# Kernel optimization log

Measured on AMD Instinct MI355X. Metric: run time of the kernel, lower is better.

Reference implementation:

```python
import jax, jax.numpy as jnp
import numpy as np

N, H, W, C = 8, 64, 64, 256
G, KS = 4, 3
K = KS * KS                      # 9 kernel points (remove_center=False)
GD = C // G                      # 64 channels per group
OM_DIM = int(np.ceil(G * K * 3 / 8) * 8)   # 112 = offsets(72)+mask(36)+pad(4)
STRIDE = PAD = DIL = 1
OFFSET_SCALE = 1.0
SOFTMAX = False


def setup_inputs() -> dict:
    ks = jax.random.split(jax.random.key(0), 6)
    s = 0.02
    return {
        "x": jax.random.normal(ks[0], (N, H * W, C), jnp.float32),
        "shape_h": H,
        "shape_w": W,
        "w_in": jax.random.normal(ks[1], (C, C), jnp.float32) * s,
        "b_in": jnp.zeros((C,), jnp.float32),
        "w_out": jax.random.normal(ks[2], (C, C), jnp.float32) * s,
        "b_out": jnp.zeros((C,), jnp.float32),
        "w_dw": jax.random.normal(ks[3], (KS, KS, 1, C), jnp.float32) * s,  # depthwise HWIO
        "b_dw": jnp.zeros((C,), jnp.float32),
        "w_pw": jax.random.normal(ks[4], (OM_DIM, C), jnp.float32) * s,
        "b_pw": jnp.zeros((OM_DIM,), jnp.float32),
    }


def _deform_sample(xg, px, py, mask):
    # xg: [N, H*W, G, GD]; px/py/mask: [N, H, W, G, K]
    # Bilinear sample with zero padding outside the image, mask-weighted sum over K.
    n_idx = jnp.arange(N)[:, None, None, None, None]
    g_idx = jnp.arange(G)[None, None, None, :, None]
    x0 = jnp.floor(px)
    y0 = jnp.floor(py)
    out = jnp.zeros((N, H, W, G, GD), xg.dtype)
    for dy in (0, 1):
        for dx in (0, 1):
            xi = x0 + dx
            yi = y0 + dy
            wgt = (1.0 - jnp.abs(px - xi)) * (1.0 - jnp.abs(py - yi))
            valid = (xi >= 0) & (xi <= W - 1) & (yi >= 0) & (yi <= H - 1)
            wgt = jnp.where(valid, wgt, 0.0) * mask                     # [N,H,W,G,K]
            flat = (jnp.clip(yi, 0, H - 1) * W + jnp.clip(xi, 0, W - 1)).astype(jnp.int32)
            vals = xg[n_idx, flat, g_idx, :]                            # [N,H,W,G,K,GD]
            out = out + jnp.einsum("nhwgk,nhwgkc->nhwgc", wgt, vals)
    return out


def _forward(x, w_in, b_in, w_out, b_out, w_dw, b_dw, w_pw, b_pw):
    out = x @ w_in.T + b_in                                             # proj_input [N,L,C]
    # offset/mask branch runs on the raw (unprojected) input
    dw = jax.lax.conv_general_dilated(
        x.reshape(N, H, W, C), w_dw, (1, 1), [(PAD, PAD), (PAD, PAD)],
        dimension_numbers=("NHWC", "HWIO", "NHWC"), feature_group_count=C) + b_dw
    om = (dw.reshape(N, H * W, C) @ w_pw.T + b_pw).reshape(N, H, W, OM_DIM)
    off = om[..., : 2 * G * K].reshape(N, H, W, G, K, 2)                # (dx, dy)
    mask = om[..., 2 * G * K : 3 * G * K].reshape(N, H, W, G, K)
    if SOFTMAX:
        mask = jax.nn.softmax(mask, axis=-1)
    # sampling locations in input pixel coordinates (DCNv3 reference points)
    kk = (jnp.arange(KS) - (KS - 1) // 2) * DIL
    kgy, kgx = jnp.meshgrid(kk, kk, indexing="ij")
    kgx = kgx.reshape(-1).astype(x.dtype)                               # [K]
    kgy = kgy.reshape(-1).astype(x.dtype)
    base = (DIL * (KS - 1)) // 2 - PAD
    bx = (jnp.arange(W) * STRIDE + base).astype(x.dtype)
    by = (jnp.arange(H) * STRIDE + base).astype(x.dtype)
    px = bx[None, None, :, None, None] + OFFSET_SCALE * (kgx + off[..., 0])
    py = by[None, :, None, None, None] + OFFSET_SCALE * (kgy + off[..., 1])
    samp = _deform_sample(out.reshape(N, H * W, G, GD), px, py, mask)   # [N,H,W,G,GD]
    return samp.reshape(N, H * W, C) @ w_out.T + b_out                  # proj_output


def reference(x, shape_h, shape_w, w_in, b_in, w_out, b_out, w_dw, b_dw, w_pw, b_pw):
    assert (shape_h, shape_w) == (H, W)
    return _forward(x, w_in, b_in, w_out, b_out, w_dw, b_dw, w_pw, b_pw)
```

## Files before the change

### kernel.cpp

```cpp
#include <hip/hip_runtime.h>

#define HW     4096
#define M_ROWS 32768
#define OMD    112
#define OMP    128

typedef __attribute__((ext_vector_type(8))) short short8;
typedef __attribute__((ext_vector_type(4))) float f32x4;

__device__ inline unsigned short f2bf(float f) {
  union { float f; unsigned int u; } v; v.f = f;
  unsigned int u = v.u;
  u += 0x7fffu + ((u >> 16) & 1u);
  return (unsigned short)(u >> 16);
}
__device__ inline float bf2f(unsigned short h) {
  union { unsigned int u; float f; } v; v.u = ((unsigned int)h) << 16;
  return v.f;
}

__global__ __launch_bounds__(256) void prep_fused(
    const float* __restrict__ x, const float* __restrict__ w_dw,
    const float* __restrict__ b_dw, const float* __restrict__ w_in,
    const float* __restrict__ w_out, const float* __restrict__ w_pw,
    const float* __restrict__ b_pw, unsigned short* __restrict__ xb,
    unsigned short* __restrict__ dwb, unsigned short* __restrict__ wi_b,
    unsigned short* __restrict__ wo_b, unsigned short* __restrict__ wp_b,
    float* __restrict__ bpw_pad) {
  int bid = blockIdx.x;
  int tid = threadIdx.x;
  if (bid < 8192) {
    int idx = bid * 256 + tid;
    int c4 = (idx & 63) * 4;
    int pp = idx >> 6;
    int n = pp >> 12;
    int hw = pp & 4095;
    int h = hw >> 6, w = hw & 63;
    float4 bb = *(const float4*)&b_dw[c4];
    float a0 = bb.x, a1 = bb.y, a2 = bb.z, a3 = bb.w;
#pragma unroll
    for (int ky = 0; ky < 3; ++ky) {
      int iy = h + ky - 1;
      if (iy < 0 || iy > 63) continue;
#pragma unroll
      for (int kx = 0; kx < 3; ++kx) {
        int ix = w + kx - 1;
        if (ix < 0 || ix > 63) continue;
        float4 xv = *(const float4*)&x[((size_t)(n << 12) + iy * 64 + ix) * 256 + c4];
        float4 wv = *(const float4*)&w_dw[(ky * 3 + kx) * 256 + c4];
        a0 += xv.x * wv.x;
        a1 += xv.y * wv.y;
        a2 += xv.z * wv.z;
        a3 += xv.w * wv.w;
      }
    }
    ushort4 o;
    o.x = f2bf(a0); o.y = f2bf(a1); o.z = f2bf(a2); o.w = f2bf(a3);
    *(ushort4*)&dwb[(size_t)pp * 256 + c4] = o;
    float4 cv = *(const float4*)&x[(size_t)pp * 256 + c4];
    ushort4 oc;
    oc.x = f2bf(cv.x); oc.y = f2bf(cv.y); oc.z = f2bf(cv.z); oc.w = f2bf(cv.w);
    *(ushort4*)&xb[(size_t)pp * 256 + c4] = oc;
  } else {
    int idx = (bid - 8192) * 256 + tid;
    if (idx < 65536) {
      wi_b[idx] = f2bf(w_in[idx]);
    } else if (idx < 131072) {
      int i = idx - 65536;
      wo_b[i] = f2bf(w_out[i]);
    } else if (idx < 131072 + OMP * 256) {
      int i = idx - 131072;
      int o = i >> 8;
      wp_b[i] = (o < OMD) ? f2bf(w_pw[i]) : (unsigned short)0;
    } else if (idx < 131072 + OMP * 256 + OMP) {
      int i = idx - (131072 + OMP * 256);
      bpw_pad[i] = (i < OMD) ? b_pw[i] : 0.f;
    }
  }
}

__global__ __launch_bounds__(256) void gemm_mid(
    const unsigned short* __restrict__ dwb, const unsigned short* __restrict__ wp_b,
    const float* __restrict__ bpw, unsigned short* __restrict__ om,
    const unsigned short* __restrict__ xb, const unsigned short* __restrict__ wi_b,
    const float* __restrict__ b_in, unsigned short* __restrict__ vproj) {
  __shared__ __align__(16) unsigned short As[128 * 32];
  __shared__ __align__(16) unsigned short Bs[128 * 32];
  int tid = threadIdx.x;
  int wave = tid >> 6, lane = tid & 63;
  int wr = wave >> 1, wc = wave & 1;

  const unsigned short *A, *W;
  const float* bias;
  unsigned short* Cout;
  int NN, colB;
  size_t rowB;
  int bid = blockIdx.x;
  if (bid < 256) {
    int swz = (bid & 7) * 32 + (bid >> 3);
    A = dwb; W = wp_b; bias = bpw; Cout = om; NN = 128;
    rowB = (size_t)swz * 128; colB = 0;
  } else {
    int b = bid - 256;
    int swz = (b & 7) * 64 + (b >> 3);
    A = xb; W = wi_b; bias = b_in; Cout = vproj; NN = 256;
    rowB = (size_t)(swz >> 1) * 128; colB = (swz & 1) * 128;
  }

  f32x4 acc[4][4];
#pragma unroll
  for (int m = 0; m < 4; ++m)
#pragma unroll
    for (int n = 0; n < 4; ++n) acc[m][n] = (f32x4)(0.f);

  int arow = lane >> 2;
  int acol = (lane & 3) * 8;

  for (int k0 = 0; k0 < 256; k0 += 32) {
#pragma unroll
    for (int jj = 0; jj < 2; ++jj) {
      int j = wave * 2 + jj;
      const unsigned short* ga = A + (rowB + 16 * j + arow) * 256 + k0 + acol;
      __builtin_amdgcn_global_load_lds(
          (const __attribute__((address_space(1))) unsigned int*)ga,
          (__attribute__((address_space(3))) unsigned int*)(As + j * 512),
          16, 0, 0);
      const unsigned short* gb =
          W + ((size_t)(colB + 16 * j + arow)) * 256 + k0 + acol;
      __builtin_amdgcn_global_load_lds(
          (const __attribute__((address_space(1))) unsigned int*)gb,
          (__attribute__((address_space(3))) unsigned int*)(Bs + j * 512),
          16, 0, 0);
    }
    __syncthreads();

    short8 aF[4], bF[4];
#pragma unroll
    for (int m = 0; m < 4; ++m)
      aF[m] = *(const short8*)&As[(wr * 64 + m * 16 + (lane & 15)) * 32 +
                                  (lane >> 4) * 8];
#pragma unroll
    for (int n = 0; n < 4; ++n)
      bF[n] = *(const short8*)&Bs[(wc * 64 + n * 16 + (lane & 15)) * 32 +
                                  (lane >> 4) * 8];
#pragma unroll
    for (int m = 0; m < 4; ++m)
#pragma unroll
      for (int n = 0; n < 4; ++n)
        acc[m][n] = __builtin_amdgcn_mfma_f32_16x16x32_bf16(
            aF[m], bF[n], acc[m][n], 0, 0, 0);
    __syncthreads();
  }

#pragma unroll
  for (int n = 0; n < 4; ++n) {
    int col = colB + wc * 64 + n * 16 + (lane & 15);
    float bv = bias[col];
#pragma unroll
    for (int m = 0; m < 4; ++m) {
#pragma unroll
      for (int j = 0; j < 4; ++j) {
        size_t row = rowB + wr * 64 + m * 16 + (lane >> 4) * 4 + j;
        Cout[row * NN + col] = f2bf(acc[m][n][j] + bv);
      }
    }
  }
}

__global__ __launch_bounds__(256) void deform_sample_v4(
    const unsigned short* __restrict__ vproj, const unsigned short* __restrict__ om,
    unsigned short* __restrict__ samp) {
  __shared__ __align__(16) unsigned short s_v[144 * 128];

  int bid = blockIdx.x;
  int swz = (bid & 7) * 128 + (bid >> 3);
  int n = swz >> 7;
  int t = swz & 127;
  int c0 = (t & 1) << 7;
  int tile = t >> 1;
  int ty0 = (tile >> 3) << 3, tx0 = (tile & 7) << 3;
  int wy0 = ty0 - 2, wx0 = tx0 - 2;

  int tid = threadIdx.x;
  int wave = tid >> 6, lane = tid & 63;

  const unsigned short* vimg = vproj + ((size_t)n << 12) * 256;
#pragma unroll
  for (int i = 0; i < 9; ++i) {
    int cell = i * 16 + (tid >> 4);
    int r = cell / 12, c = cell % 12;
    int gy = min(max(wy0 + r, 0), 63);
    int gx = min(max(wx0 + c, 0), 63);
    const unsigned short* src =
        vimg + (size_t)(gy * 64 + gx) * 256 + c0 + (tid & 15) * 8;
    __builtin_amdgcn_global_load_lds(
        (const __attribute__((address_space(1))) unsigned int*)src,
        (__attribute__((address_space(3))) unsigned int*)(s_v + i * 2048 + wave * 512),
        16, 0, 0);
  }
  __syncthreads();

  int sub = lane & 15;
  int g = (c0 >> 6) + (sub >> 3);
  int chlds = sub * 8;

#pragma unroll
  for (int iter = 0; iter < 4; ++iter) {
    int pl = iter * 16 + wave * 4 + (lane >> 4);
    int py = pl >> 3, pxx = pl & 7;
    int hy = ty0 + py, wx = tx0 + pxx;
    int p = (n << 12) + hy * 64 + wx;
    const unsigned short* o = om + (size_t)p * OMP;

    float acc[8];
#pragma unroll
    for (int j = 0; j < 8; ++j) acc[j] = 0.f;

#pragma unroll
    for (int k = 0; k < 9; ++k) {
      int gk = g * 9 + k;
      float ox = bf2f(o[gk * 2]), oy = bf2f(o[gk * 2 + 1]);
      float msk = bf2f(o[72 + gk]);
      float px = (float)(wx + (k % 3) - 1) + ox;
      float py2 = (float)(hy + (k / 3) - 1) + oy;
      float x0f = floorf(px), y0f = floorf(py2);
      int x0 = (int)x0f, y0 = (int)y0f;
      float fx = px - x0f, fy = py2 - y0f;
      bool vx0 = (unsigned)x0 < 64u, vx1 = (unsigned)(x0 + 1) < 64u;
      bool vy0 = (unsigned)y0 < 64u, vy1 = (unsigned)(y0 + 1) < 64u;
      float w00 = (vy0 && vx0) ? (1.f - fx) * (1.f - fy) * msk : 0.f;
      float w01 = (vy0 && vx1) ? fx * (1.f - fy) * msk : 0.f;
      float w10 = (vy1 && vx0) ? (1.f - fx) * fy * msk : 0.f;
      float w11 = (vy1 && vx1) ? fx * fy * msk : 0.f;
      int ix0 = min(max(min(max(x0, 0), 63) - wx0, 0), 11);
      int ix1 = min(max(min(max(x0 + 1, 0), 63) - wx0, 0), 11);
      int iy0 = min(max(min(max(y0, 0), 63) - wy0, 0), 11);
      int iy1 = min(max(min(max(y0 + 1, 0), 63) - wy0, 0), 11);
      short8 v00 = *(const short8*)&s_v[(iy0 * 12 + ix0) * 128 + chlds];
      short8 v01 = *(const short8*)&s_v[(iy0 * 12 + ix1) * 128 + chlds];
      short8 v10 = *(const short8*)&s_v[(iy1 * 12 + ix0) * 128 + chlds];
      short8 v11 = *(const short8*)&s_v[(iy1 * 12 + ix1) * 128 + chlds];
#pragma unroll
      for (int j = 0; j < 8; ++j)
        acc[j] += w00 * bf2f((unsigned short)v00[j]) +
                  w01 * bf2f((unsigned short)v01[j]) +
                  w10 * bf2f((unsigned short)v10[j]) +
                  w11 * bf2f((unsigned short)v11[j]);
    }

    union { unsigned short s[8]; short8 v8; } o8;
#pragma unroll
    for (int j = 0; j < 8; ++j) o8.s[j] = f2bf(acc[j]);
    *(short8*)&samp[(size_t)p * 256 + c0 + sub * 8] = o8.v8;
  }
}

__global__ __launch_bounds__(256) void gemm_out(
    const unsigned short* __restrict__ A, const unsigned short* __restrict__ W,
    const float* __restrict__ bias, float* __restrict__ Cout) {
  __shared__ __align__(16) unsigned short As[128 * 32];
  __shared__ __align__(16) unsigned short Bs[128 * 32];
  int tid = threadIdx.x;
  int wave = tid >> 6, lane = tid & 63;
  int wr = wave >> 1, wc = wave & 1;

  int bid = blockIdx.x;
  int swz = (bid & 7) * 64 + (bid >> 3);
  size_t rowB = (size_t)(swz >> 1) * 128;
  int colB = (swz & 1) * 128;

  f32x4 acc[4][4];
#pragma unroll
  for (int m = 0; m < 4; ++m)
#pragma unroll
    for (int n = 0; n < 4; ++n) acc[m][n] = (f32x4)(0.f);

  int arow = lane >> 2;
  int acol = (lane & 3) * 8;

  for (int k0 = 0; k0 < 256; k0 += 32) {
#pragma unroll
    for (int jj = 0; jj < 2; ++jj) {
      int j = wave * 2 + jj;
      const unsigned short* ga = A + (rowB + 16 * j + arow) * 256 + k0 + acol;
      __builtin_amdgcn_global_load_lds(
          (const __attribute__((address_space(1))) unsigned int*)ga,
          (__attribute__((address_space(3))) unsigned int*)(As + j * 512),
          16, 0, 0);
      const unsigned short* gb =
          W + ((size_t)(colB + 16 * j + arow)) * 256 + k0 + acol;
      __builtin_amdgcn_global_load_lds(
          (const __attribute__((address_space(1))) unsigned int*)gb,
          (__attribute__((address_space(3))) unsigned int*)(Bs + j * 512),
          16, 0, 0);
    }
    __syncthreads();

    short8 aF[4], bF[4];
#pragma unroll
    for (int m = 0; m < 4; ++m)
      aF[m] = *(const short8*)&As[(wr * 64 + m * 16 + (lane & 15)) * 32 +
                                  (lane >> 4) * 8];
#pragma unroll
    for (int n = 0; n < 4; ++n)
      bF[n] = *(const short8*)&Bs[(wc * 64 + n * 16 + (lane & 15)) * 32 +
                                  (lane >> 4) * 8];
#pragma unroll
    for (int m = 0; m < 4; ++m)
#pragma unroll
      for (int n = 0; n < 4; ++n)
        acc[m][n] = __builtin_amdgcn_mfma_f32_16x16x32_bf16(
            aF[m], bF[n], acc[m][n], 0, 0, 0);
    __syncthreads();
  }

#pragma unroll
  for (int n = 0; n < 4; ++n) {
    int col = colB + wc * 64 + n * 16 + (lane & 15);
    float bv = bias[col];
#pragma unroll
    for (int m = 0; m < 4; ++m) {
#pragma unroll
      for (int j = 0; j < 4; ++j) {
        size_t row = rowB + wr * 64 + m * 16 + (lane >> 4) * 4 + j;
        Cout[row * 256 + col] = acc[m][n][j] + bv;
      }
    }
  }
}

extern "C" void kernel_launch(void* const* d_in, const int* in_sizes, int n_in,
                              void* d_out, int out_size, void* d_ws,
                              size_t ws_size, hipStream_t stream) {
  const float* x     = (const float*)d_in[0];
  const float* w_in  = (const float*)d_in[3];
  const float* b_in  = (const float*)d_in[4];
  const float* w_out = (const float*)d_in[5];
  const float* b_out = (const float*)d_in[6];
  const float* w_dw  = (const float*)d_in[7];
  const float* b_dw  = (const float*)d_in[8];
  const float* w_pw  = (const float*)d_in[9];
  const float* b_pw  = (const float*)d_in[10];
  float* out = (float*)d_out;
  char* ws = (char*)d_ws;

  unsigned short* xb    = (unsigned short*)(ws);
  unsigned short* dwb   = (unsigned short*)(ws + (16u << 20));
  unsigned short* vproj = (unsigned short*)(ws + (32u << 20));
  unsigned short* om    = (unsigned short*)(ws + (48u << 20));
  unsigned short* wi_b  = (unsigned short*)(ws + (56u << 20));
  unsigned short* wo_b  = (unsigned short*)(ws + (56u << 20) + (128u << 10));
  unsigned short* wp_b  = (unsigned short*)(ws + (56u << 20) + (256u << 10));
  float*          bpw   = (float*)(ws + (56u << 20) + (320u << 10));

  prep_fused<<<8834, 256, 0, stream>>>(x, w_dw, b_dw, w_in, w_out, w_pw, b_pw,
                                       xb, dwb, wi_b, wo_b, wp_b, bpw);
  gemm_mid<<<768, 256, 0, stream>>>(dwb, wp_b, bpw, om, xb, wi_b, b_in, vproj);
  deform_sample_v4<<<1024, 256, 0, stream>>>(vproj, om, dwb );
  gemm_out<<<512, 256, 0, stream>>>(dwb, wo_b, b_out, out);
}
```

Baseline: 92.45 us.

## Precompute bilinear weights and offsets per block in LDS, split blocks by group

```diff
diff --git a/kernel.cpp b/kernel.cpp
--- a/kernel.cpp
+++ b/kernel.cpp
@@ -167,17 +167,19 @@
   }
 }
 
-__global__ __launch_bounds__(256) void deform_sample_v4(
+__global__ __launch_bounds__(256) void deform_sample_v5(
     const unsigned short* __restrict__ vproj, const unsigned short* __restrict__ om,
     unsigned short* __restrict__ samp) {
-  __shared__ __align__(16) unsigned short s_v[144 * 128];
+  __shared__ __align__(16) unsigned short s_v[144 * 64];
+  __shared__ __align__(16) float4 s_wgt[576];
+  __shared__ __align__(16) int4   s_off[576];
 
   int bid = blockIdx.x;
-  int swz = (bid & 7) * 128 + (bid >> 3);
-  int n = swz >> 7;
-  int t = swz & 127;
-  int c0 = (t & 1) << 7;
-  int tile = t >> 1;
+  int swz = (bid & 7) * 256 + (bid >> 3);
+  int n = swz >> 8;
+  int rem = swz & 255;
+  int tile = rem >> 2;
+  int g = rem & 3;
   int ty0 = (tile >> 3) << 3, tx0 = (tile & 7) << 3;
   int wy0 = ty0 - 2, wx0 = tx0 - 2;
 
@@ -185,32 +187,69 @@
   int wave = tid >> 6, lane = tid & 63;
 
   const unsigned short* vimg = vproj + ((size_t)n << 12) * 256;
-#pragma unroll
-  for (int i = 0; i < 9; ++i) {
-    int cell = i * 16 + (tid >> 4);
-    int r = cell / 12, c = cell % 12;
-    int gy = min(max(wy0 + r, 0), 63);
-    int gx = min(max(wx0 + c, 0), 63);
-    const unsigned short* src =
-        vimg + (size_t)(gy * 64 + gx) * 256 + c0 + (tid & 15) * 8;
-    __builtin_amdgcn_global_load_lds(
-        (const __attribute__((address_space(1))) unsigned int*)src,
-        (__attribute__((address_space(3))) unsigned int*)(s_v + i * 2048 + wave * 512),
-        16, 0, 0);
+
+#pragma unroll
+  for (int i = 0; i < 5; ++i) {
+    int seg = i * 4 + wave;
+    if (seg < 18) {
+      int f = seg * 1024 + lane * 16;
+      int cell = f >> 7;
+      int inner = (f >> 1) & 63;
+      int r = cell / 12, c = cell - r * 12;
+      int gy = min(max(wy0 + r, 0), 63);
+      int gx = min(max(wx0 + c, 0), 63);
+      const unsigned short* src =
+          vimg + (size_t)(gy * 64 + gx) * 256 + g * 64 + inner;
+      __builtin_amdgcn_global_load_lds(
+          (const __attribute__((address_space(1))) unsigned int*)src,
+          (__attribute__((address_space(3))) unsigned int*)(s_v + seg * 512),
+          16, 0, 0);
+    }
+  }
+
+  for (int e = tid; e < 576; e += 256) {
+    int pl = e / 9, k = e - pl * 9;
+    int hy = ty0 + (pl >> 3), wx = tx0 + (pl & 7);
+    int p = (n << 12) + hy * 64 + wx;
+    int gk = g * 9 + k;
+    const unsigned short* o = om + (size_t)p * OMP;
+    float ox = bf2f(o[gk * 2]), oy = bf2f(o[gk * 2 + 1]);
+    float msk = bf2f(o[72 + gk]);
+    float px = (float)(wx + (k % 3) - 1) + ox;
+    float py = (float)(hy + (k / 3) - 1) + oy;
+    float x0f = floorf(px), y0f = floorf(py);
+    int x0 = (int)x0f, y0 = (int)y0f;
+    float fx = px - x0f, fy = py - y0f;
+    bool vx0 = (unsigned)x0 < 64u, vx1 = (unsigned)(x0 + 1) < 64u;
+    bool vy0 = (unsigned)y0 < 64u, vy1 = (unsigned)(y0 + 1) < 64u;
+    float4 wv;
+    wv.x = (vy0 && vx0) ? (1.f - fx) * (1.f - fy) * msk : 0.f;
+    wv.y = (vy0 && vx1) ? fx * (1.f - fy) * msk : 0.f;
+    wv.z = (vy1 && vx0) ? (1.f - fx) * fy * msk : 0.f;
+    wv.w = (vy1 && vx1) ? fx * fy * msk : 0.f;
+    int ix0 = min(max(min(max(x0, 0), 63) - wx0, 0), 11);
+    int ix1 = min(max(min(max(x0 + 1, 0), 63) - wx0, 0), 11);
+    int iy0 = min(max(min(max(y0, 0), 63) - wy0, 0), 11);
+    int iy1 = min(max(min(max(y0 + 1, 0), 63) - wy0, 0), 11);
+    int4 ov;
+    ov.x = (iy0 * 12 + ix0) * 128;
+    ov.y = (iy0 * 12 + ix1) * 128;
+    ov.z = (iy1 * 12 + ix0) * 128;
+    ov.w = (iy1 * 12 + ix1) * 128;
+    s_wgt[e] = wv;
+    s_off[e] = ov;
   }
   __syncthreads();
 
-  int sub = lane & 15;
-  int g = (c0 >> 6) + (sub >> 3);
-  int chlds = sub * 8;
-
-#pragma unroll
-  for (int iter = 0; iter < 4; ++iter) {
-    int pl = iter * 16 + wave * 4 + (lane >> 4);
-    int py = pl >> 3, pxx = pl & 7;
-    int hy = ty0 + py, wx = tx0 + pxx;
+  int sub = lane & 7;
+  int chb = sub * 16;
+  const char* vb = (const char*)s_v;
+
+#pragma unroll
+  for (int iter = 0; iter < 2; ++iter) {
+    int pl = iter * 32 + wave * 8 + (lane >> 3);
+    int hy = ty0 + (pl >> 3), wx = tx0 + (pl & 7);
     int p = (n << 12) + hy * 64 + wx;
-    const unsigned short* o = om + (size_t)p * OMP;
 
     float acc[8];
 #pragma unroll
@@ -218,40 +257,25 @@
 
 #pragma unroll
     for (int k = 0; k < 9; ++k) {
-      int gk = g * 9 + k;
-      float ox = bf2f(o[gk * 2]), oy = bf2f(o[gk * 2 + 1]);
-      float msk = bf2f(o[72 + gk]);
-      float px = (float)(wx + (k % 3) - 1) + ox;
-      float py2 = (float)(hy + (k / 3) - 1) + oy;
-      float x0f = floorf(px), y0f = floorf(py2);
-      int x0 = (int)x0f, y0 = (int)y0f;
-      float fx = px - x0f, fy = py2 - y0f;
-      bool vx0 = (unsigned)x0 < 64u, vx1 = (unsigned)(x0 + 1) < 64u;
-      bool vy0 = (unsigned)y0 < 64u, vy1 = (unsigned)(y0 + 1) < 64u;
-      float w00 = (vy0 && vx0) ? (1.f - fx) * (1.f - fy) * msk : 0.f;
-      float w01 = (vy0 && vx1) ? fx * (1.f - fy) * msk : 0.f;
-      float w10 = (vy1 && vx0) ? (1.f - fx) * fy * msk : 0.f;
-      float w11 = (vy1 && vx1) ? fx * fy * msk : 0.f;
-      int ix0 = min(max(min(max(x0, 0), 63) - wx0, 0), 11);
-      int ix1 = min(max(min(max(x0 + 1, 0), 63) - wx0, 0), 11);
-      int iy0 = min(max(min(max(y0, 0), 63) - wy0, 0), 11);
-      int iy1 = min(max(min(max(y0 + 1, 0), 63) - wy0, 0), 11);
-      short8 v00 = *(const short8*)&s_v[(iy0 * 12 + ix0) * 128 + chlds];
-      short8 v01 = *(const short8*)&s_v[(iy0 * 12 + ix1) * 128 + chlds];
-      short8 v10 = *(const short8*)&s_v[(iy1 * 12 + ix0) * 128 + chlds];
-      short8 v11 = *(const short8*)&s_v[(iy1 * 12 + ix1) * 128 + chlds];
+      int e = pl * 9 + k;
+      float4 wv = s_wgt[e];
+      int4 ov = s_off[e];
+      short8 v00 = *(const short8*)(vb + ov.x + chb);
+      short8 v01 = *(const short8*)(vb + ov.y + chb);
+      short8 v10 = *(const short8*)(vb + ov.z + chb);
+      short8 v11 = *(const short8*)(vb + ov.w + chb);
 #pragma unroll
       for (int j = 0; j < 8; ++j)
-        acc[j] += w00 * bf2f((unsigned short)v00[j]) +
-                  w01 * bf2f((unsigned short)v01[j]) +
-                  w10 * bf2f((unsigned short)v10[j]) +
-                  w11 * bf2f((unsigned short)v11[j]);
+        acc[j] += wv.x * bf2f((unsigned short)v00[j]) +
+                  wv.y * bf2f((unsigned short)v01[j]) +
+                  wv.z * bf2f((unsigned short)v10[j]) +
+                  wv.w * bf2f((unsigned short)v11[j]);
     }
 
     union { unsigned short s[8]; short8 v8; } o8;
 #pragma unroll
     for (int j = 0; j < 8; ++j) o8.s[j] = f2bf(acc[j]);
-    *(short8*)&samp[(size_t)p * 256 + c0 + sub * 8] = o8.v8;
+    *(short8*)&samp[(size_t)p * 256 + g * 64 + sub * 8] = o8.v8;
   }
 }
 
@@ -356,6 +380,6 @@
   prep_fused<<<8834, 256, 0, stream>>>(x, w_dw, b_dw, w_in, w_out, w_pw, b_pw,
                                        xb, dwb, wi_b, wo_b, wp_b, bpw);
   gemm_mid<<<768, 256, 0, stream>>>(dwb, wp_b, bpw, om, xb, wi_b, b_in, vproj);
-  deform_sample_v4<<<1024, 256, 0, stream>>>(vproj, om, dwb );
+  deform_sample_v5<<<2048, 256, 0, stream>>>(vproj, om, dwb );
   gemm_out<<<512, 256, 0, stream>>>(dwb, wo_b, b_out, out);
 }
```

Result: faster. 81.42 us (-11.9%).
